# Kernel optimization log

Measured on AMD Instinct MI355X. Metric: run time of the kernel, lower is better.

## Reference

```python
import jax, jax.numpy as jnp
import numpy as np

R = 4            # message-passing rounds
D = 128          # embedding dim
NUM_VARS = 100000
NUM_LITS = 2 * NUM_VARS
NUM_CLAUSES = 420000
NNZ = 3 * NUM_CLAUSES  # 3-SAT: 3 literals per clause

def _w(k, shape):
    # Kaiming-ish init so 4 rounds of MLPs stay numerically sane.
    return (jax.random.normal(k, shape, jnp.float32) / np.sqrt(shape[-2])).astype(jnp.float32)

def setup_inputs() -> dict:
    ks = jax.random.split(jax.random.key(0), 16)
    return {
        "edge_clause": jax.random.randint(ks[0], (NNZ,), 0, NUM_CLAUSES, dtype=jnp.int32),
        "edge_lit":    jax.random.randint(ks[1], (NNZ,), 0, NUM_LITS, dtype=jnp.int32),
        "c_W1": _w(ks[2], (R, 2 * D, D)), "c_b1": jnp.zeros((R, D), jnp.float32),
        "c_W2": _w(ks[3], (R, D, D)),     "c_b2": jnp.zeros((R, D), jnp.float32),
        "l_W1": _w(ks[4], (R, 3 * D, D)), "l_b1": jnp.zeros((R, D), jnp.float32),
        "l_W2": _w(ks[5], (R, D, D)),     "l_b2": jnp.zeros((R, D), jnp.float32),
        "v_W1": _w(ks[6], (2 * D, D)), "v_b1": jnp.zeros((D,), jnp.float32),
        "v_W2": _w(ks[7], (D, D)),     "v_b2": jnp.zeros((D,), jnp.float32),
        "v_W3": _w(ks[8], (D, D)),     "v_b3": jnp.zeros((D,), jnp.float32),
        "v_W4": _w(ks[9], (D, 1)),     "v_b4": jnp.zeros((1,), jnp.float32),
        "c_init_scale": jnp.float32(1.0 / np.sqrt(D)),
        "l_init_scale": jnp.float32(1.0 / np.sqrt(D)),
        "lc_scale": jnp.float32(0.1),
        "cl_scale": jnp.float32(0.1),
        "num_clauses": NUM_CLAUSES,
        "num_lits": NUM_LITS,
    }

def reference(edge_clause, edge_lit, c_W1, c_b1, c_W2, c_b2, l_W1, l_b1, l_W2, l_b2,
              v_W1, v_b1, v_W2, v_b2, v_W3, v_b3, v_W4, v_b4,
              c_init_scale, l_init_scale, lc_scale, cl_scale, num_clauses, num_lits):
    d = c_b1.shape[-1]
    num_vars = num_lits // 2
    num_rounds = c_W1.shape[0]
    L = jnp.ones((num_lits, d), jnp.float32) * l_init_scale      # literal embeddings
    C = jnp.ones((num_clauses, d), jnp.float32) * c_init_scale   # clause embeddings
    for r in range(num_rounds):
        # LC_msgs = G @ L  (COO SpMM via gather + segment_sum over clauses)
        LC = jax.ops.segment_sum(L[edge_lit], edge_clause, num_segments=num_clauses) * lc_scale
        h = jax.nn.relu(jnp.concatenate([C, LC], -1) @ c_W1[r] + c_b1[r])
        C = h @ c_W2[r] + c_b2[r]
        # CL_msgs = G^T @ C
        CL = jax.ops.segment_sum(C[edge_clause], edge_lit, num_segments=num_lits) * cl_scale
        flipL = jnp.concatenate([L[num_vars:], L[:num_vars]], 0)  # negated-literal pairing
        h = jax.nn.relu(jnp.concatenate([L, CL, flipL], -1) @ l_W1[r] + l_b1[r])
        L = h @ l_W2[r] + l_b2[r]
    V = jnp.concatenate([L[:num_vars], L[num_vars:]], -1)  # [num_vars, 2d]
    h = jax.nn.relu(V @ v_W1 + v_b1)
    h = jax.nn.relu(h @ v_W2 + v_b2)
    h = jax.nn.relu(h @ v_W3 + v_b3)
    return jnp.squeeze(h @ v_W4 + v_b4, -1)  # [num_vars]
```

## Files before the change

kernel.cpp:

```cpp
#include <hip/hip_runtime.h>
#include <hip/hip_bf16.h>
#include <hip/hip_fp16.h>
#include <cstddef>


#define NVv 100000
#define NLv 200000
#define NCv 420000
#define NNZv 1260000
#define Dv 128

#define WS_NEEDED 225882368ULL

typedef _Float16 half8 __attribute__((ext_vector_type(8)));
typedef float f32x4 __attribute__((ext_vector_type(4)));
#define MFMA16(a, b, c) __builtin_amdgcn_mfma_f32_16x16x32_f16(a, b, c, 0, 0, 0)

__device__ __forceinline__ void ldh8(const __half* p, float* o) {
  uint4 v = *(const uint4*)p;
  const __half2* h = (const __half2*)&v;
#pragma unroll
  for (int i = 0; i < 4; i++) {
    float2 f = __half22float2(h[i]);
    o[2 * i] = f.x;
    o[2 * i + 1] = f.y;
  }
}

__global__ __launch_bounds__(256) void zero_ints(int* __restrict__ p, int n) {
  int i = blockIdx.x * 256 + threadIdx.x;
  if (i < n) p[i] = 0;
}

__global__ __launch_bounds__(256) void fill_out(float* __restrict__ p, int n,
                                                float val) {
  int i = blockIdx.x * 256 + threadIdx.x;
  if (i < n) p[i] = val;
}

__global__ __launch_bounds__(256) void fill_val(float* __restrict__ p, long long n4,
                                                const float* __restrict__ sp) {
  float s = *sp;
  float4 v = make_float4(s, s, s, s);
  long long i = (long long)blockIdx.x * blockDim.x + threadIdx.x;
  long long stride = (long long)gridDim.x * blockDim.x;
  for (; i < n4; i += stride) ((float4*)p)[i] = v;
}

__global__ __launch_bounds__(256) void fill_half(__half2* __restrict__ p, long long n2,
                                                 const float* __restrict__ sp) {
  __half2 v = __float2half2_rn(*sp);
  long long i = (long long)blockIdx.x * blockDim.x + threadIdx.x;
  long long stride = (long long)gridDim.x * blockDim.x;
  for (; i < n2; i += stride) p[i] = v;
}

__global__ __launch_bounds__(256) void conv_w(const float* __restrict__ src,
                                              __half* __restrict__ dst, int K) {
  int i = blockIdx.x * 256 + threadIdx.x;
  if (i >= K * 128) return;
  int k = i >> 7, n = i & 127;
  dst[n * K + k] = __float2half(src[i]);
}

__global__ __launch_bounds__(256) void hist_kernel(const int* __restrict__ ec,
                                                   const int* __restrict__ el,
                                                   int* __restrict__ cnt_c,
                                                   int* __restrict__ cnt_l, int nnz) {
  int e = blockIdx.x * blockDim.x + threadIdx.x;
  if (e >= nnz) return;
  atomicAdd(&cnt_c[ec[e]], 1);
  atomicAdd(&cnt_l[el[e]], 1);
}

__global__ __launch_bounds__(256) void scan_block(const int* __restrict__ in, int n,
                                                  int* __restrict__ out,
                                                  int* __restrict__ bsums) {
  __shared__ int s[256];
  int tid = threadIdx.x;
  int base = blockIdx.x * 1024 + tid * 4;
  int v[4];
  int tsum = 0;
#pragma unroll
  for (int j = 0; j < 4; j++) {
    int x = (base + j < n) ? in[base + j] : 0;
    v[j] = tsum;
    tsum += x;
  }
  s[tid] = tsum;
  __syncthreads();
  for (int off = 1; off < 256; off <<= 1) {
    int x = 0;
    if (tid >= off) x = s[tid - off];
    __syncthreads();
    s[tid] += x;
    __syncthreads();
  }
  int excl = s[tid] - tsum;
#pragma unroll
  for (int j = 0; j < 4; j++)
    if (base + j < n) out[base + j] = v[j] + excl;
  if (tid == 255 && bsums) bsums[blockIdx.x] = s[255];
}

__global__ __launch_bounds__(256) void add_offsets(int* __restrict__ out,
                                                   const int* __restrict__ bo, int n) {
  int i = blockIdx.x * 256 + threadIdx.x;
  if (i < n) out[i] += bo[i >> 10];
}

__global__ void set_tail(int* a, int va, int* b, int vb) {
  a[0] = va;
  b[0] = vb;
}

__global__ __launch_bounds__(256) void fill_csr(const int* __restrict__ ec,
                                                const int* __restrict__ el,
                                                const int* __restrict__ rpc,
                                                const int* __restrict__ rpl,
                                                int* __restrict__ cnt_c,
                                                int* __restrict__ cnt_l,
                                                int* __restrict__ col_c,
                                                int* __restrict__ col_l, int nnz) {
  int e = blockIdx.x * blockDim.x + threadIdx.x;
  if (e >= nnz) return;
  int c = ec[e], l = el[e];
  col_c[rpc[c] + atomicAdd(&cnt_c[c], 1)] = l;
  col_l[rpl[l] + atomicAdd(&cnt_l[l], 1)] = c;
}

__global__ __launch_bounds__(256) void clause_mfma(
    const float* __restrict__ Lsrc, __half* __restrict__ C,
    const int* __restrict__ rpc, const int* __restrict__ colc,
    const __half* __restrict__ W1t, const float* __restrict__ b1,
    const __half* __restrict__ W2t, const float* __restrict__ b2,
    const float* __restrict__ lc_sp) {
  __shared__ __half ACt[64 * 256];
  __shared__ __half Bst[128 * 32];
  const int tid = threadIdx.x;
  const int row0 = blockIdx.x * 64;
  const int lane = tid & 63, wid = tid >> 6;
  const int wrow = wid * 16;
  const int R = lane & 15, kb = lane >> 4;
  const float lc_scale = *lc_sp;

  {
    int r = tid >> 2, q = tid & 3;
    int grow = row0 + r;
    grow = grow < NCv ? grow : NCv - 1;
    const uint4* csrc = (const uint4*)(C + (size_t)grow * Dv + q * 32);
#pragma unroll
    for (int j = 0; j < 4; j++) {
      unsigned byte = (unsigned)(r * 512 + q * 64 + j * 16) ^ ((r & 7) << 4);
      *(uint4*)((char*)ACt + byte) = csrc[j];
    }
    int s = rpc[grow], e = rpc[grow + 1];
    float a[32];
#pragma unroll
    for (int t = 0; t < 32; t++) a[t] = 0.f;
    for (int i = s; i < e; ++i) {
      const float* src = Lsrc + (size_t)colc[i] * Dv + q * 32;
#pragma unroll
      for (int t = 0; t < 8; t++) {
        float4 v = *(const float4*)(src + t * 4);
        a[t * 4 + 0] += v.x;
        a[t * 4 + 1] += v.y;
        a[t * 4 + 2] += v.z;
        a[t * 4 + 3] += v.w;
      }
    }
#pragma unroll
    for (int j = 0; j < 4; j++) {
      union { __half h[8]; uint4 u; } tmp;
#pragma unroll
      for (int t = 0; t < 8; t++) tmp.h[t] = __float2half(a[j * 8 + t] * lc_scale);
      unsigned byte = (unsigned)(r * 512 + 256 + q * 64 + j * 16) ^ ((r & 7) << 4);
      *(uint4*)((char*)ACt + byte) = tmp.u;
    }
  }

  f32x4 acc[8];
#pragma unroll
  for (int t = 0; t < 8; t++) acc[t] = (f32x4){0.f, 0.f, 0.f, 0.f};

  for (int ks = 0; ks < 8; ks++) {
    {
      int n = tid >> 1, part = tid & 1;
      const uint4* wsrc = (const uint4*)(W1t + (size_t)n * 256 + ks * 32 + part * 16);
#pragma unroll
      for (int jj = 0; jj < 2; jj++) {
        unsigned byte = (unsigned)(n * 64 + (part * 2 + jj) * 16) ^ ((n & 3) << 4);
        *(uint4*)((char*)Bst + byte) = wsrc[jj];
      }
    }
    __syncthreads();
    unsigned abyte =
        (unsigned)((wrow + R) * 512 + ks * 64 + kb * 16) ^ ((R & 7) << 4);
    half8 af = *(const half8*)((const char*)ACt + abyte);
#pragma unroll
    for (int nt = 0; nt < 8; nt++) {
      int n = nt * 16 + R;
      unsigned bbyte = (unsigned)(n * 64 + kb * 16) ^ ((n & 3) << 4);
      half8 bf = *(const half8*)((const char*)Bst + bbyte);
      acc[nt] = MFMA16(af, bf, acc[nt]);
    }
    __syncthreads();
  }

#pragma unroll
  for (int nt = 0; nt < 8; nt++) {
    int col = nt * 16 + R;
    float bv = b1[col];
#pragma unroll
    for (int r2 = 0; r2 < 4; r2++) {
      int row = wrow + kb * 4 + r2;
      float hv = fmaxf(acc[nt][r2] + bv, 0.f);
      unsigned byte = (unsigned)(row * 512 + col * 2) ^ ((row & 7) << 4);
      *(__half*)((char*)ACt + byte) = __float2half(hv);
    }
  }
  __syncthreads();

  f32x4 acc2[8];
#pragma unroll
  for (int t = 0; t < 8; t++) acc2[t] = (f32x4){0.f, 0.f, 0.f, 0.f};

  for (int ks = 0; ks < 4; ks++) {
    {
      int n = tid >> 1, part = tid & 1;
      const uint4* wsrc = (const uint4*)(W2t + (size_t)n * 128 + ks * 32 + part * 16);
#pragma unroll
      for (int jj = 0; jj < 2; jj++) {
        unsigned byte = (unsigned)(n * 64 + (part * 2 + jj) * 16) ^ ((n & 3) << 4);
        *(uint4*)((char*)Bst + byte) = wsrc[jj];
      }
    }
    __syncthreads();
    unsigned abyte =
        (unsigned)((wrow + R) * 512 + ks * 64 + kb * 16) ^ ((R & 7) << 4);
    half8 af = *(const half8*)((const char*)ACt + abyte);
#pragma unroll
    for (int nt = 0; nt < 8; nt++) {
      int n = nt * 16 + R;
      unsigned bbyte = (unsigned)(n * 64 + kb * 16) ^ ((n & 3) << 4);
      half8 bf = *(const half8*)((const char*)Bst + bbyte);
      acc2[nt] = MFMA16(af, bf, acc2[nt]);
    }
    __syncthreads();
  }

#pragma unroll
  for (int nt = 0; nt < 8; nt++) {
    int col = nt * 16 + R;
    float bv = b2[col];
#pragma unroll
    for (int r2 = 0; r2 < 4; r2++) {
      int row = row0 + wrow + kb * 4 + r2;
      if (row < NCv) C[(size_t)row * Dv + col] = __float2half(acc2[nt][r2] + bv);
    }
  }
}

__global__ __launch_bounds__(256) void lit_mfma(
    float* __restrict__ L, const __half* __restrict__ C,
    const int* __restrict__ rpl, const int* __restrict__ coll,
    const __half* __restrict__ W1t, const float* __restrict__ b1,
    const __half* __restrict__ W2t, const float* __restrict__ b2,
    const float* __restrict__ cl_sp) {
  __shared__ __half ALt[64 * 256];
  __shared__ __half Bst[128 * 32];
  const int tid = threadIdx.x;
  const int p0 = blockIdx.x * 32;
  const int lane = tid & 63, wid = tid >> 6;
  const int wrow = wid * 16;
  const int R = lane & 15, kb = lane >> 4;
  const float cl_scale = *cl_sp;

  {
    int r = tid >> 2, q = tid & 3;
    int gl = (r < 32) ? (p0 + r) : (NVv + p0 + (r - 32));
    const float* lsrc = L + (size_t)gl * Dv + q * 32;
#pragma unroll
    for (int j = 0; j < 4; j++) {
      float4 v0 = *(const float4*)(lsrc + j * 8);
      float4 v1 = *(const float4*)(lsrc + j * 8 + 4);
      union { __half h[8]; uint4 u; } tmp;
      tmp.h[0] = __float2half(v0.x);
      tmp.h[1] = __float2half(v0.y);
      tmp.h[2] = __float2half(v0.z);
      tmp.h[3] = __float2half(v0.w);
      tmp.h[4] = __float2half(v1.x);
      tmp.h[5] = __float2half(v1.y);
      tmp.h[6] = __float2half(v1.z);
      tmp.h[7] = __float2half(v1.w);
      unsigned byte = (unsigned)(r * 512 + q * 64 + j * 16) ^ ((r & 7) << 4);
      *(uint4*)((char*)ALt + byte) = tmp.u;
    }
    int s = rpl[gl], e = rpl[gl + 1];
    float a[32];
#pragma unroll
    for (int t = 0; t < 32; t++) a[t] = 0.f;
    for (int i = s; i < e; ++i) {
      const __half* src = C + (size_t)coll[i] * Dv + q * 32;
#pragma unroll
      for (int t = 0; t < 4; t++) {
        float o[8];
        ldh8(src + t * 8, o);
#pragma unroll
        for (int j = 0; j < 8; j++) a[t * 8 + j] += o[j];
      }
    }
#pragma unroll
    for (int j = 0; j < 4; j++) {
      union { __half h[8]; uint4 u; } tmp;
#pragma unroll
      for (int t = 0; t < 8; t++) tmp.h[t] = __float2half(a[j * 8 + t] * cl_scale);
      unsigned byte = (unsigned)(r * 512 + 256 + q * 64 + j * 16) ^ ((r & 7) << 4);
      *(uint4*)((char*)ALt + byte) = tmp.u;
    }
  }

  f32x4 acc[8];
#pragma unroll
  for (int t = 0; t < 8; t++) acc[t] = (f32x4){0.f, 0.f, 0.f, 0.f};

  for (int ks = 0; ks < 12; ks++) {
    {
      int n = tid >> 1, part = tid & 1;
      const uint4* wsrc = (const uint4*)(W1t + (size_t)n * 384 + ks * 32 + part * 16);
#pragma unroll
      for (int jj = 0; jj < 2; jj++) {
        unsigned byte = (unsigned)(n * 64 + (part * 2 + jj) * 16) ^ ((n & 3) << 4);
        *(uint4*)((char*)Bst + byte) = wsrc[jj];
      }
    }
    __syncthreads();
    int arow = wrow + R;
    int acol = ks * 64;
    if (ks >= 8) {
      arow ^= 32;
      acol = (ks - 8) * 64;
    }
    unsigned abyte = (unsigned)(arow * 512 + acol + kb * 16) ^ ((R & 7) << 4);
    half8 af = *(const half8*)((const char*)ALt + abyte);
#pragma unroll
    for (int nt = 0; nt < 8; nt++) {
      int n = nt * 16 + R;
      unsigned bbyte = (unsigned)(n * 64 + kb * 16) ^ ((n & 3) << 4);
      half8 bf = *(const half8*)((const char*)Bst + bbyte);
      acc[nt] = MFMA16(af, bf, acc[nt]);
    }
    __syncthreads();
  }

#pragma unroll
  for (int nt = 0; nt < 8; nt++) {
    int col = nt * 16 + R;
    float bv = b1[col];
#pragma unroll
    for (int r2 = 0; r2 < 4; r2++) {
      int row = wrow + kb * 4 + r2;
      float hv = fmaxf(acc[nt][r2] + bv, 0.f);
      unsigned byte = (unsigned)(row * 512 + col * 2) ^ ((row & 7) << 4);
      *(__half*)((char*)ALt + byte) = __float2half(hv);
    }
  }
  __syncthreads();

  f32x4 acc2[8];
#pragma unroll
  for (int t = 0; t < 8; t++) acc2[t] = (f32x4){0.f, 0.f, 0.f, 0.f};

  for (int ks = 0; ks < 4; ks++) {
    {
      int n = tid >> 1, part = tid & 1;
      const uint4* wsrc = (const uint4*)(W2t + (size_t)n * 128 + ks * 32 + part * 16);
#pragma unroll
      for (int jj = 0; jj < 2; jj++) {
        unsigned byte = (unsigned)(n * 64 + (part * 2 + jj) * 16) ^ ((n & 3) << 4);
        *(uint4*)((char*)Bst + byte) = wsrc[jj];
      }
    }
    __syncthreads();
    unsigned abyte =
        (unsigned)((wrow + R) * 512 + ks * 64 + kb * 16) ^ ((R & 7) << 4);
    half8 af = *(const half8*)((const char*)ALt + abyte);
#pragma unroll
    for (int nt = 0; nt < 8; nt++) {
      int n = nt * 16 + R;
      unsigned bbyte = (unsigned)(n * 64 + kb * 16) ^ ((n & 3) << 4);
      half8 bf = *(const half8*)((const char*)Bst + bbyte);
      acc2[nt] = MFMA16(af, bf, acc2[nt]);
    }
    __syncthreads();
  }

#pragma unroll
  for (int nt = 0; nt < 8; nt++) {
    int col = nt * 16 + R;
    float bv = b2[col];
#pragma unroll
    for (int r2 = 0; r2 < 4; r2++) {
      int lr = wrow + kb * 4 + r2;
      int gl = (lr < 32) ? (p0 + lr) : (NVv + p0 + (lr - 32));
      L[(size_t)gl * Dv + col] = acc2[nt][r2] + bv;
    }
  }
}

template <int MODE>
__device__ __forceinline__ const float* a_row(const float* __restrict__ A0, int row,
                                              int kblk, int half) {
  if (MODE == 0) return A0 + (size_t)row * Dv;
  return A0 + (size_t)(kblk == 0 ? row : row + half) * Dv;
}

template <int MODE>
__global__ __launch_bounds__(256) void gemm_tiled(const float* __restrict__ A0,
                                                  const float* __restrict__ B,
                                                  const float* __restrict__ bias,
                                                  float* __restrict__ Out, int M, int K,
                                                  int do_relu, int half) {
  __shared__ float As[32][132];
  __shared__ float Bs[32][128];
  const int tid = threadIdx.x;
  const int row0 = blockIdx.x * 128;
  const int ty4 = (tid >> 4) * 4;
  const int tx4 = (tid & 15) * 4;
  const int arow = tid >> 3;
  const int ak4 = (tid & 7) * 4;

  float accf[8][8];
#pragma unroll
  for (int i = 0; i < 8; i++)
#pragma unroll
    for (int j = 0; j < 8; j++) accf[i][j] = 0.f;

  for (int k0 = 0; k0 < K; k0 += 32) {
#pragma unroll
    for (int p = 0; p < 4; ++p) {
      int r = p * 32 + arow;
      int grow = row0 + r;
      grow = grow < M ? grow : M - 1;
      int gk = k0 + ak4;
      const float* ap = a_row<MODE>(A0, grow, gk >> 7, half);
      float4 v = *(const float4*)(ap + (gk & 127));
      As[ak4 + 0][r] = v.x;
      As[ak4 + 1][r] = v.y;
      As[ak4 + 2][r] = v.z;
      As[ak4 + 3][r] = v.w;
    }
    {
      const int bk = tid >> 3;
      const int n0 = (tid & 7) * 4;
      const float* bp = B + (size_t)(k0 + bk) * 128 + n0;
#pragma unroll
      for (int j = 0; j < 4; j++) {
        float4 v = *(const float4*)(bp + j * 32);
        *(float4*)&Bs[bk][n0 + j * 32] = v;
      }
    }
    __syncthreads();
#pragma unroll
    for (int k = 0; k < 32; k++) {
      float4 a0 = *(const float4*)&As[k][ty4];
      float4 a1 = *(const float4*)&As[k][ty4 + 64];
      float4 b0 = *(const float4*)&Bs[k][tx4];
      float4 b1 = *(const float4*)&Bs[k][tx4 + 64];
      float ar[8] = {a0.x, a0.y, a0.z, a0.w, a1.x, a1.y, a1.z, a1.w};
      float br[8] = {b0.x, b0.y, b0.z, b0.w, b1.x, b1.y, b1.z, b1.w};
#pragma unroll
      for (int i = 0; i < 8; i++)
#pragma unroll
        for (int j = 0; j < 8; j++) accf[i][j] = fmaf(ar[i], br[j], accf[i][j]);
    }
    __syncthreads();
  }

  float bv[8];
#pragma unroll
  for (int j = 0; j < 8; j++) bv[j] = bias[(j < 4) ? tx4 + j : tx4 + 60 + j];
#pragma unroll
  for (int i = 0; i < 8; i++) {
    int r = row0 + ((i < 4) ? ty4 + i : ty4 + 60 + i);
    if (r >= M) continue;
    float o[8];
#pragma unroll
    for (int j = 0; j < 8; j++) {
      float v = accf[i][j] + bv[j];
      o[j] = do_relu ? fmaxf(v, 0.f) : v;
    }
    *(float4*)&Out[(size_t)r * 128 + tx4] = make_float4(o[0], o[1], o[2], o[3]);
    *(float4*)&Out[(size_t)r * 128 + tx4 + 64] = make_float4(o[4], o[5], o[6], o[7]);
  }
}

__global__ __launch_bounds__(256) void matvec(const float* __restrict__ A,
                                              const float* __restrict__ w,
                                              const float* __restrict__ b,
                                              float* __restrict__ out, int M) {
  int r = blockIdx.x * 4 + (threadIdx.x >> 6);
  int lane = threadIdx.x & 63;
  if (r >= M) return;
  float2 a = *(const float2*)&A[(size_t)r * Dv + lane * 2];
  float2 wv = *(const float2*)&w[lane * 2];
  float s = a.x * wv.x + a.y * wv.y;
#pragma unroll
  for (int off = 32; off > 0; off >>= 1) s += __shfl_down(s, off, 64);
  if (lane == 0) out[r] = s + b[0];
}

extern "C" void kernel_launch(void* const* d_in, const int* in_sizes, int n_in,
                              void* d_out, int out_size, void* d_ws, size_t ws_size,
                              hipStream_t stream) {
  float* out = (float*)d_out;

  if (ws_size < (size_t)WS_NEEDED) {
    fill_out<<<(out_size + 255) / 256, 256, 0, stream>>>(out, out_size,
                                                         (float)(ws_size >> 20));
    return;
  }

  const int* edge_clause = (const int*)d_in[0];
  const int* edge_lit = (const int*)d_in[1];
  const float* c_W1 = (const float*)d_in[2];
  const float* c_b1 = (const float*)d_in[3];
  const float* c_W2 = (const float*)d_in[4];
  const float* c_b2 = (const float*)d_in[5];
  const float* l_W1 = (const float*)d_in[6];
  const float* l_b1 = (const float*)d_in[7];
  const float* l_W2 = (const float*)d_in[8];
  const float* l_b2 = (const float*)d_in[9];
  const float* v_W1 = (const float*)d_in[10];
  const float* v_b1 = (const float*)d_in[11];
  const float* v_W2 = (const float*)d_in[12];
  const float* v_b2 = (const float*)d_in[13];
  const float* v_W3 = (const float*)d_in[14];
  const float* v_b3 = (const float*)d_in[15];
  const float* v_W4 = (const float*)d_in[16];
  const float* v_b4 = (const float*)d_in[17];
  const float* c_init = (const float*)d_in[18];
  const float* l_init = (const float*)d_in[19];
  const float* lc_s = (const float*)d_in[20];
  const float* cl_s = (const float*)d_in[21];

  char* p = (char*)d_ws;
  auto alloc = [&](size_t b) -> void* {
    void* r = (void*)p;
    p += (b + 255) & ~(size_t)255;
    return r;
  };
  float* Lbuf = (float*)alloc((size_t)NLv * Dv * 4);
  __half* Cbuf = (__half*)alloc((size_t)NCv * Dv * 2);
  int* rpc = (int*)alloc((size_t)(NCv + 1) * 4);
  int* rpl = (int*)alloc((size_t)(NLv + 1) * 4);
  int* cnt_c = (int*)alloc((size_t)NCv * 4);
  int* cnt_l = (int*)alloc((size_t)NLv * 4);
  int* col_c = (int*)alloc((size_t)NNZv * 4);
  int* col_l = (int*)alloc((size_t)NNZv * 4);
  int* bs1 = (int*)alloc(512 * 4);
  int* bs2 = (int*)alloc(512 * 4);
  __half* cW1t = (__half*)alloc((size_t)4 * 128 * 256 * 2);
  __half* cW2t = (__half*)alloc((size_t)4 * 128 * 128 * 2);
  __half* lW1t = (__half*)alloc((size_t)4 * 128 * 384 * 2);
  __half* lW2t = (__half*)alloc((size_t)4 * 128 * 128 * 2);

  const int gzc = (NCv + 255) / 256, gzl = (NLv + 255) / 256;

  for (int r = 0; r < 4; r++) {
    conv_w<<<128, 256, 0, stream>>>(c_W1 + (size_t)r * 256 * 128,
                                    cW1t + (size_t)r * 128 * 256, 256);
    conv_w<<<64, 256, 0, stream>>>(c_W2 + (size_t)r * 128 * 128,
                                   cW2t + (size_t)r * 128 * 128, 128);
    conv_w<<<192, 256, 0, stream>>>(l_W1 + (size_t)r * 384 * 128,
                                    lW1t + (size_t)r * 128 * 384, 384);
    conv_w<<<64, 256, 0, stream>>>(l_W2 + (size_t)r * 128 * 128,
                                   lW2t + (size_t)r * 128 * 128, 128);
  }

  zero_ints<<<gzc, 256, 0, stream>>>(cnt_c, NCv);
  zero_ints<<<gzl, 256, 0, stream>>>(cnt_l, NLv);
  fill_val<<<2048, 256, 0, stream>>>(Lbuf, (long long)NLv * (Dv / 4), l_init);
  fill_half<<<2048, 256, 0, stream>>>((__half2*)Cbuf, (long long)NCv * (Dv / 2),
                                      c_init);
  hist_kernel<<<(NNZv + 255) / 256, 256, 0, stream>>>(edge_clause, edge_lit, cnt_c,
                                                      cnt_l, NNZv);
  int nb_c = (NCv + 1023) / 1024;
  scan_block<<<nb_c, 256, 0, stream>>>(cnt_c, NCv, rpc, bs1);
  scan_block<<<1, 256, 0, stream>>>(bs1, nb_c, bs1, nullptr);
  add_offsets<<<gzc, 256, 0, stream>>>(rpc, bs1, NCv);
  int nb_l = (NLv + 1023) / 1024;
  scan_block<<<nb_l, 256, 0, stream>>>(cnt_l, NLv, rpl, bs2);
  scan_block<<<1, 256, 0, stream>>>(bs2, nb_l, bs2, nullptr);
  add_offsets<<<gzl, 256, 0, stream>>>(rpl, bs2, NLv);
  set_tail<<<1, 1, 0, stream>>>(rpc + NCv, NNZv, rpl + NLv, NNZv);
  zero_ints<<<gzc, 256, 0, stream>>>(cnt_c, NCv);
  zero_ints<<<gzl, 256, 0, stream>>>(cnt_l, NLv);
  fill_csr<<<(NNZv + 255) / 256, 256, 0, stream>>>(edge_clause, edge_lit, rpc, rpl,
                                                   cnt_c, cnt_l, col_c, col_l, NNZv);

  const int gCf = (NCv + 63) / 64;
  const int gLf = NVv / 32;
  for (int r = 0; r < 4; r++) {
    clause_mfma<<<gCf, 256, 0, stream>>>(
        Lbuf, Cbuf, rpc, col_c, cW1t + (size_t)r * 128 * 256,
        c_b1 + (size_t)r * 128, cW2t + (size_t)r * 128 * 128,
        c_b2 + (size_t)r * 128, lc_s);
    lit_mfma<<<gLf, 256, 0, stream>>>(
        Lbuf, Cbuf, rpl, col_l, lW1t + (size_t)r * 128 * 384,
        l_b1 + (size_t)r * 128, lW2t + (size_t)r * 128 * 128,
        l_b2 + (size_t)r * 128, cl_s);
  }

  float* h1 = (float*)Cbuf;
  float* h2 = h1 + (size_t)NVv * Dv;
  const int gV = (NVv + 127) / 128;
  gemm_tiled<3><<<gV, 256, 0, stream>>>(Lbuf, v_W1, v_b1, h1, NVv, 256, 1, NVv);
  gemm_tiled<0><<<gV, 256, 0, stream>>>(h1, v_W2, v_b2, h2, NVv, 128, 1, 0);
  gemm_tiled<0><<<gV, 256, 0, stream>>>(h2, v_W3, v_b3, h1, NVv, 128, 1, 0);
  matvec<<<(NVv + 3) / 4, 256, 0, stream>>>(h1, v_W4, v_b4, out, NVv);
}
```

Measured before the change: 2.086 ms.

## Store literal embeddings in fp16 and run readout MLP on MFMA

Literal embeddings are now kept in half precision, which halves the gather traffic in the clause aggregation and removes the fp32-to-fp16 conversion in the literal kernel. The three fp32 SIMT tiled GEMMs of the variable readout MLP are replaced with fp16 MFMA kernels fed by pre-transposed half weights, and the final matvec reads half activations. This trades extra rounding error in L and the readout activations for lower memory bandwidth and matrix-core throughput.

```diff
diff --git a/kernel.cpp b/kernel.cpp
--- a/kernel.cpp
+++ b/kernel.cpp
@@ -10,7 +10,7 @@
 #define NNZv 1260000
 #define Dv 128
 
-#define WS_NEEDED 225882368ULL
+#define WS_NEEDED 174813440ULL
 
 typedef _Float16 half8 __attribute__((ext_vector_type(8)));
 typedef float f32x4 __attribute__((ext_vector_type(4)));
@@ -36,15 +36,6 @@
                                                 float val) {
   int i = blockIdx.x * 256 + threadIdx.x;
   if (i < n) p[i] = val;
-}
-
-__global__ __launch_bounds__(256) void fill_val(float* __restrict__ p, long long n4,
-                                                const float* __restrict__ sp) {
-  float s = *sp;
-  float4 v = make_float4(s, s, s, s);
-  long long i = (long long)blockIdx.x * blockDim.x + threadIdx.x;
-  long long stride = (long long)gridDim.x * blockDim.x;
-  for (; i < n4; i += stride) ((float4*)p)[i] = v;
 }
 
 __global__ __launch_bounds__(256) void fill_half(__half2* __restrict__ p, long long n2,
@@ -130,7 +121,7 @@
 }
 
 __global__ __launch_bounds__(256) void clause_mfma(
-    const float* __restrict__ Lsrc, __half* __restrict__ C,
+    const __half* __restrict__ Lsrc, __half* __restrict__ C,
     const int* __restrict__ rpc, const int* __restrict__ colc,
     const __half* __restrict__ W1t, const float* __restrict__ b1,
     const __half* __restrict__ W2t, const float* __restrict__ b2,
@@ -159,14 +150,13 @@
 #pragma unroll
     for (int t = 0; t < 32; t++) a[t] = 0.f;
     for (int i = s; i < e; ++i) {
-      const float* src = Lsrc + (size_t)colc[i] * Dv + q * 32;
-#pragma unroll
-      for (int t = 0; t < 8; t++) {
-        float4 v = *(const float4*)(src + t * 4);
-        a[t * 4 + 0] += v.x;
-        a[t * 4 + 1] += v.y;
-        a[t * 4 + 2] += v.z;
-        a[t * 4 + 3] += v.w;
+      const __half* src = Lsrc + (size_t)colc[i] * Dv + q * 32;
+#pragma unroll
+      for (int t = 0; t < 4; t++) {
+        float o[8];
+        ldh8(src + t * 8, o);
+#pragma unroll
+        for (int j = 0; j < 8; j++) a[t * 8 + j] += o[j];
       }
     }
 #pragma unroll
@@ -262,7 +252,7 @@
 }
 
 __global__ __launch_bounds__(256) void lit_mfma(
-    float* __restrict__ L, const __half* __restrict__ C,
+    __half* __restrict__ L, const __half* __restrict__ C,
     const int* __restrict__ rpl, const int* __restrict__ coll,
     const __half* __restrict__ W1t, const float* __restrict__ b1,
     const __half* __restrict__ W2t, const float* __restrict__ b2,
@@ -279,22 +269,11 @@
   {
     int r = tid >> 2, q = tid & 3;
     int gl = (r < 32) ? (p0 + r) : (NVv + p0 + (r - 32));
-    const float* lsrc = L + (size_t)gl * Dv + q * 32;
+    const uint4* lsrc = (const uint4*)(L + (size_t)gl * Dv + q * 32);
 #pragma unroll
     for (int j = 0; j < 4; j++) {
-      float4 v0 = *(const float4*)(lsrc + j * 8);
-      float4 v1 = *(const float4*)(lsrc + j * 8 + 4);
-      union { __half h[8]; uint4 u; } tmp;
-      tmp.h[0] = __float2half(v0.x);
-      tmp.h[1] = __float2half(v0.y);
-      tmp.h[2] = __float2half(v0.z);
-      tmp.h[3] = __float2half(v0.w);
-      tmp.h[4] = __float2half(v1.x);
-      tmp.h[5] = __float2half(v1.y);
-      tmp.h[6] = __float2half(v1.z);
-      tmp.h[7] = __float2half(v1.w);
       unsigned byte = (unsigned)(r * 512 + q * 64 + j * 16) ^ ((r & 7) << 4);
-      *(uint4*)((char*)ALt + byte) = tmp.u;
+      *(uint4*)((char*)ALt + byte) = lsrc[j];
     }
     int s = rpl[gl], e = rpl[gl + 1];
     float a[32];
@@ -403,106 +382,94 @@
     for (int r2 = 0; r2 < 4; r2++) {
       int lr = wrow + kb * 4 + r2;
       int gl = (lr < 32) ? (p0 + lr) : (NVv + p0 + (lr - 32));
-      L[(size_t)gl * Dv + col] = acc2[nt][r2] + bv;
+      L[(size_t)gl * Dv + col] = __float2half(acc2[nt][r2] + bv);
     }
   }
 }
 
 template <int MODE>
-__device__ __forceinline__ const float* a_row(const float* __restrict__ A0, int row,
-                                              int kblk, int half) {
-  if (MODE == 0) return A0 + (size_t)row * Dv;
-  return A0 + (size_t)(kblk == 0 ? row : row + half) * Dv;
-}
-
-template <int MODE>
-__global__ __launch_bounds__(256) void gemm_tiled(const float* __restrict__ A0,
-                                                  const float* __restrict__ B,
-                                                  const float* __restrict__ bias,
-                                                  float* __restrict__ Out, int M, int K,
-                                                  int do_relu, int half) {
-  __shared__ float As[32][132];
-  __shared__ float Bs[32][128];
+__global__ __launch_bounds__(256) void gemm_mfma(const __half* __restrict__ A,
+                                                 const __half* __restrict__ Wt,
+                                                 const float* __restrict__ bias,
+                                                 __half* __restrict__ Out, int M) {
+  constexpr int K = (MODE == 3) ? 256 : 128;
+  constexpr int RS = K * 2;
+  __shared__ __half ALt[64 * K];
+  __shared__ __half Bst[128 * 32];
   const int tid = threadIdx.x;
-  const int row0 = blockIdx.x * 128;
-  const int ty4 = (tid >> 4) * 4;
-  const int tx4 = (tid & 15) * 4;
-  const int arow = tid >> 3;
-  const int ak4 = (tid & 7) * 4;
-
-  float accf[8][8];
-#pragma unroll
-  for (int i = 0; i < 8; i++)
-#pragma unroll
-    for (int j = 0; j < 8; j++) accf[i][j] = 0.f;
-
-  for (int k0 = 0; k0 < K; k0 += 32) {
-#pragma unroll
-    for (int p = 0; p < 4; ++p) {
-      int r = p * 32 + arow;
-      int grow = row0 + r;
-      grow = grow < M ? grow : M - 1;
-      int gk = k0 + ak4;
-      const float* ap = a_row<MODE>(A0, grow, gk >> 7, half);
-      float4 v = *(const float4*)(ap + (gk & 127));
-      As[ak4 + 0][r] = v.x;
-      As[ak4 + 1][r] = v.y;
-      As[ak4 + 2][r] = v.z;
-      As[ak4 + 3][r] = v.w;
-    }
+  const int row0 = blockIdx.x * 64;
+  const int lane = tid & 63, wid = tid >> 6;
+  const int wrow = wid * 16;
+  const int R = lane & 15, kb = lane >> 4;
+
+  {
+    int r = tid >> 2, q = tid & 3;
+    int grow = row0 + r;
+    grow = grow < M ? grow : M - 1;
+    const uint4* s0 = (const uint4*)(A + (size_t)grow * Dv + q * 32);
+#pragma unroll
+    for (int j = 0; j < 4; j++) {
+      unsigned byte = (unsigned)(r * RS + q * 64 + j * 16) ^ ((r & 7) << 4);
+      *(uint4*)((char*)ALt + byte) = s0[j];
+    }
+    if (MODE == 3) {
+      const uint4* s1 = (const uint4*)(A + (size_t)(NVv + grow) * Dv + q * 32);
+#pragma unroll
+      for (int j = 0; j < 4; j++) {
+        unsigned byte = (unsigned)(r * RS + 256 + q * 64 + j * 16) ^ ((r & 7) << 4);
+        *(uint4*)((char*)ALt + byte) = s1[j];
+      }
+    }
+  }
+
+  f32x4 acc[8];
+#pragma unroll
+  for (int t = 0; t < 8; t++) acc[t] = (f32x4){0.f, 0.f, 0.f, 0.f};
+
+  for (int ks = 0; ks < K / 32; ks++) {
     {
-      const int bk = tid >> 3;
-      const int n0 = (tid & 7) * 4;
-      const float* bp = B + (size_t)(k0 + bk) * 128 + n0;
-#pragma unroll
-      for (int j = 0; j < 4; j++) {
-        float4 v = *(const float4*)(bp + j * 32);
-        *(float4*)&Bs[bk][n0 + j * 32] = v;
-      }
-    }
-    __syncthreads();
-#pragma unroll
-    for (int k = 0; k < 32; k++) {
-      float4 a0 = *(const float4*)&As[k][ty4];
-      float4 a1 = *(const float4*)&As[k][ty4 + 64];
-      float4 b0 = *(const float4*)&Bs[k][tx4];
-      float4 b1 = *(const float4*)&Bs[k][tx4 + 64];
-      float ar[8] = {a0.x, a0.y, a0.z, a0.w, a1.x, a1.y, a1.z, a1.w};
-      float br[8] = {b0.x, b0.y, b0.z, b0.w, b1.x, b1.y, b1.z, b1.w};
-#pragma unroll
-      for (int i = 0; i < 8; i++)
-#pragma unroll
-        for (int j = 0; j < 8; j++) accf[i][j] = fmaf(ar[i], br[j], accf[i][j]);
-    }
-    __syncthreads();
-  }
-
-  float bv[8];
-#pragma unroll
-  for (int j = 0; j < 8; j++) bv[j] = bias[(j < 4) ? tx4 + j : tx4 + 60 + j];
-#pragma unroll
-  for (int i = 0; i < 8; i++) {
-    int r = row0 + ((i < 4) ? ty4 + i : ty4 + 60 + i);
-    if (r >= M) continue;
-    float o[8];
-#pragma unroll
-    for (int j = 0; j < 8; j++) {
-      float v = accf[i][j] + bv[j];
-      o[j] = do_relu ? fmaxf(v, 0.f) : v;
-    }
-    *(float4*)&Out[(size_t)r * 128 + tx4] = make_float4(o[0], o[1], o[2], o[3]);
-    *(float4*)&Out[(size_t)r * 128 + tx4 + 64] = make_float4(o[4], o[5], o[6], o[7]);
-  }
-}
-
-__global__ __launch_bounds__(256) void matvec(const float* __restrict__ A,
-                                              const float* __restrict__ w,
-                                              const float* __restrict__ b,
-                                              float* __restrict__ out, int M) {
+      int n = tid >> 1, part = tid & 1;
+      const uint4* wsrc = (const uint4*)(Wt + (size_t)n * K + ks * 32 + part * 16);
+#pragma unroll
+      for (int jj = 0; jj < 2; jj++) {
+        unsigned byte = (unsigned)(n * 64 + (part * 2 + jj) * 16) ^ ((n & 3) << 4);
+        *(uint4*)((char*)Bst + byte) = wsrc[jj];
+      }
+    }
+    __syncthreads();
+    unsigned abyte = (unsigned)((wrow + R) * RS + ks * 64 + kb * 16) ^ ((R & 7) << 4);
+    half8 af = *(const half8*)((const char*)ALt + abyte);
+#pragma unroll
+    for (int nt = 0; nt < 8; nt++) {
+      int n = nt * 16 + R;
+      unsigned bbyte = (unsigned)(n * 64 + kb * 16) ^ ((n & 3) << 4);
+      half8 bf = *(const half8*)((const char*)Bst + bbyte);
+      acc[nt] = MFMA16(af, bf, acc[nt]);
+    }
+    __syncthreads();
+  }
+
+#pragma unroll
+  for (int nt = 0; nt < 8; nt++) {
+    int col = nt * 16 + R;
+    float bv = bias[col];
+#pragma unroll
+    for (int r2 = 0; r2 < 4; r2++) {
+      int row = row0 + wrow + kb * 4 + r2;
+      if (row < M)
+        Out[(size_t)row * Dv + col] = __float2half(fmaxf(acc[nt][r2] + bv, 0.f));
+    }
+  }
+}
+
+__global__ __launch_bounds__(256) void matvec_h(const __half* __restrict__ A,
+                                                const float* __restrict__ w,
+                                                const float* __restrict__ b,
+                                                float* __restrict__ out, int M) {
   int r = blockIdx.x * 4 + (threadIdx.x >> 6);
   int lane = threadIdx.x & 63;
   if (r >= M) return;
-  float2 a = *(const float2*)&A[(size_t)r * Dv + lane * 2];
+  float2 a = __half22float2(*(const __half2*)&A[(size_t)r * Dv + lane * 2]);
   float2 wv = *(const float2*)&w[lane * 2];
   float s = a.x * wv.x + a.y * wv.y;
 #pragma unroll
@@ -550,7 +517,7 @@
     p += (b + 255) & ~(size_t)255;
     return r;
   };
-  float* Lbuf = (float*)alloc((size_t)NLv * Dv * 4);
+  __half* Lbuf = (__half*)alloc((size_t)NLv * Dv * 2);
   __half* Cbuf = (__half*)alloc((size_t)NCv * Dv * 2);
   int* rpc = (int*)alloc((size_t)(NCv + 1) * 4);
   int* rpl = (int*)alloc((size_t)(NLv + 1) * 4);
@@ -564,6 +531,9 @@
   __half* cW2t = (__half*)alloc((size_t)4 * 128 * 128 * 2);
   __half* lW1t = (__half*)alloc((size_t)4 * 128 * 384 * 2);
   __half* lW2t = (__half*)alloc((size_t)4 * 128 * 128 * 2);
+  __half* vW1t = (__half*)alloc((size_t)128 * 256 * 2);
+  __half* vW2t = (__half*)alloc((size_t)128 * 128 * 2);
+  __half* vW3t = (__half*)alloc((size_t)128 * 128 * 2);
 
   const int gzc = (NCv + 255) / 256, gzl = (NLv + 255) / 256;
 
@@ -577,10 +547,14 @@
     conv_w<<<64, 256, 0, stream>>>(l_W2 + (size_t)r * 128 * 128,
                                    lW2t + (size_t)r * 128 * 128, 128);
   }
+  conv_w<<<128, 256, 0, stream>>>(v_W1, vW1t, 256);
+  conv_w<<<64, 256, 0, stream>>>(v_W2, vW2t, 128);
+  conv_w<<<64, 256, 0, stream>>>(v_W3, vW3t, 128);
 
   zero_ints<<<gzc, 256, 0, stream>>>(cnt_c, NCv);
   zero_ints<<<gzl, 256, 0, stream>>>(cnt_l, NLv);
-  fill_val<<<2048, 256, 0, stream>>>(Lbuf, (long long)NLv * (Dv / 4), l_init);
+  fill_half<<<2048, 256, 0, stream>>>((__half2*)Lbuf, (long long)NLv * (Dv / 2),
+                                      l_init);
   fill_half<<<2048, 256, 0, stream>>>((__half2*)Cbuf, (long long)NCv * (Dv / 2),
                                       c_init);
   hist_kernel<<<(NNZv + 255) / 256, 256, 0, stream>>>(edge_clause, edge_lit, cnt_c,
@@ -612,11 +586,11 @@
         l_b2 + (size_t)r * 128, cl_s);
   }
 
-  float* h1 = (float*)Cbuf;
-  float* h2 = h1 + (size_t)NVv * Dv;
-  const int gV = (NVv + 127) / 128;
-  gemm_tiled<3><<<gV, 256, 0, stream>>>(Lbuf, v_W1, v_b1, h1, NVv, 256, 1, NVv);
-  gemm_tiled<0><<<gV, 256, 0, stream>>>(h1, v_W2, v_b2, h2, NVv, 128, 1, 0);
-  gemm_tiled<0><<<gV, 256, 0, stream>>>(h2, v_W3, v_b3, h1, NVv, 128, 1, 0);
-  matvec<<<(NVv + 3) / 4, 256, 0, stream>>>(h1, v_W4, v_b4, out, NVv);
-}
+  __half* h1 = Cbuf;
+  __half* h2 = Cbuf + (size_t)NVv * Dv;
+  const int gVm = (NVv + 63) / 64;
+  gemm_mfma<3><<<gVm, 256, 0, stream>>>(Lbuf, vW1t, v_b1, h1, NVv);
+  gemm_mfma<0><<<gVm, 256, 0, stream>>>(h1, vW2t, v_b2, h2, NVv);
+  gemm_mfma<0><<<gVm, 256, 0, stream>>>(h2, vW3t, v_b3, h1, NVv);
+  matvec_h<<<(NVv + 3) / 4, 256, 0, stream>>>(h1, v_W4, v_b4, out, NVv);
+}
```

After: 1.703 ms. 18.4% less time.
